# Optimization experiments

Measured on AMD Instinct MI355X. Metric: run time of the kernel, lower is better.

The kernel has to match this reference:

```python
import jax, jax.numpy as jnp
import numpy as np

B, H, N, D, S = 32, 4, 8192, 64, 3
EPS = 1e-10


def setup_inputs() -> dict:
    key = jax.random.key(0)
    ks = jax.random.split(key, 9)
    dev = 1.0 / np.sqrt(D + N)  # init scale from initialize_memory()
    memory = jax.random.uniform(ks[0], (B, N, D), minval=-dev, maxval=dev, dtype=jnp.float32)
    k = jax.random.normal(ks[1], (B, H, D), dtype=jnp.float32)
    beta = jax.random.uniform(ks[2], (B, H), dtype=jnp.float32) * 5.0          # key strength >= 0
    pw = jax.nn.softmax(jax.random.normal(ks[3], (B, H, N), dtype=jnp.float32), axis=-1)  # prev weights: simplex
    g = jax.random.uniform(ks[4], (B, H), dtype=jnp.float32)                    # gate in [0,1]
    s = jax.nn.softmax(jax.random.normal(ks[5], (B, H, S), dtype=jnp.float32), axis=-1)   # shift distribution
    gamma = 1.0 + 2.0 * jax.random.uniform(ks[6], (B, H), dtype=jnp.float32)    # sharpening >= 1
    erase = jax.random.uniform(ks[7], (B, H, D), dtype=jnp.float32)             # erase in [0,1]
    add = jax.random.normal(ks[8], (B, H, D), dtype=jnp.float32)
    return {"memory": memory, "k": k, "beta": beta, "pw": pw, "g": g,
            "s": s, "gamma": gamma, "erase": erase, "add": add}


def _ntm_step(memory, k, beta, pw, g, s, gamma, erase, add):
    # --- content addressing: softmax over slots of beta * cosine similarity ---
    kn = k / (jnp.linalg.norm(k, axis=-1, keepdims=True) + EPS)         # [B,H,D]
    mn = memory / (jnp.linalg.norm(memory, axis=-1, keepdims=True) + EPS)  # [B,N,D]
    cos = jnp.einsum('bhd,bnd->bhn', kn, mn)                            # [B,H,N]
    wc = jax.nn.softmax(beta[..., None] * cos, axis=-1)
    # --- location addressing: interpolate, circular shift, sharpen ---
    gb = g[..., None]
    wg = gb * wc + (1.0 - gb) * pw                                      # [B,H,N]
    center = (s.shape[-1] - 1) // 2
    # ws(i) = sum_j wg((i - off_j) mod N) * s(j), off_j = j - center
    ws = sum(s[..., j:j + 1] * jnp.roll(wg, j - center, axis=-1)
             for j in range(s.shape[-1]))
    wgam = ws ** gamma[..., None]
    w = wgam / jnp.sum(wgam, axis=-1, keepdims=True)                    # [B,H,N]
    # --- write: sequential erase/add outer products per head ---
    mem = memory
    for h in range(w.shape[1]):
        e = w[:, h, :, None] * erase[:, h, None, :]                     # [B,N,D]
        a = w[:, h, :, None] * add[:, h, None, :]
        mem = mem * (1.0 - e) + a
    # --- read from updated memory ---
    reading = jnp.einsum('bhn,bnd->bhd', w, mem)                        # [B,H,D]
    return reading


def reference(memory, k, beta, pw, g, s, gamma, erase, add):
    return _ntm_step(memory, k, beta, pw, g, s, gamma, erase, add)
```

## Files before the change

### kernel.cpp

```cpp
#include <hip/hip_runtime.h>
#include <math.h>

#define Bc 32
#define Hc 4
#define Nc 8192
#define Dc 64
#define EPSc 1e-10f

#define T1ROWS 64
#define NT1 (Nc / T1ROWS)
#define T2ROWS 256
#define NT2 (Nc / T2ROWS)
#define T3ROWS 128
#define NT3 (Nc / T3ROWS)

__global__ __launch_bounds__(256) void k_scores(
    const float* __restrict__ mem, const float* __restrict__ kk,
    const float* __restrict__ beta,
    float* __restrict__ tbuf, float* __restrict__ z1p)
{
    const int b = blockIdx.y, tile = blockIdx.x, tid = threadIdx.x;
    const int wave = tid >> 6, lane = tid & 63;

    __shared__ float ks[Hc][Dc];
    __shared__ float wsum[4][Hc];

    {
        float kv = kk[(b * Hc + wave) * Dc + lane];
        float ss = kv * kv;
        #pragma unroll
        for (int off = 32; off; off >>= 1) ss += __shfl_xor(ss, off);
        float scale = beta[b * Hc + wave] / (sqrtf(ss) + EPSc);
        ks[wave][lane] = kv * scale;
    }
    __syncthreads();

    const int r    = tid >> 2;
    const int part = tid & 3;
    const int n    = tile * T1ROWS + r;
    const float4* p4 = reinterpret_cast<const float4*>(
        mem + ((size_t)b * Nc + n) * Dc + part * 16);

    float ss = 0.f;
    float dot[Hc] = {0.f, 0.f, 0.f, 0.f};
    #pragma unroll
    for (int j = 0; j < 4; ++j) {
        float4 v = p4[j];
        ss = fmaf(v.x, v.x, ss); ss = fmaf(v.y, v.y, ss);
        ss = fmaf(v.z, v.z, ss); ss = fmaf(v.w, v.w, ss);
        const int c0 = part * 16 + 4 * j;
        #pragma unroll
        for (int h = 0; h < Hc; ++h) {
            dot[h] = fmaf(v.x, ks[h][c0 + 0], dot[h]);
            dot[h] = fmaf(v.y, ks[h][c0 + 1], dot[h]);
            dot[h] = fmaf(v.z, ks[h][c0 + 2], dot[h]);
            dot[h] = fmaf(v.w, ks[h][c0 + 3], dot[h]);
        }
    }
    #pragma unroll
    for (int off = 1; off <= 2; off <<= 1) {
        ss += __shfl_xor(ss, off);
        #pragma unroll
        for (int h = 0; h < Hc; ++h) dot[h] += __shfl_xor(dot[h], off);
    }
    const float inv = 1.0f / (sqrtf(ss) + EPSc);

    const float tval = __expf(dot[part] * inv);
    tbuf[(b * Hc + part) * Nc + n] = tval;

    float v = tval;
    #pragma unroll
    for (int off = 4; off <= 32; off <<= 1) v += __shfl_xor(v, off);
    if (lane < Hc) wsum[wave][lane] = v;
    __syncthreads();
    if (tid < Hc)
        z1p[(b * Hc + tid) * NT1 + tile] =
            wsum[0][tid] + wsum[1][tid] + wsum[2][tid] + wsum[3][tid];
}

__global__ __launch_bounds__(256) void k_shift(
    const float* __restrict__ tbuf, const float* __restrict__ z1p,
    const float* __restrict__ pw, const float* __restrict__ g,
    const float* __restrict__ s, const float* __restrict__ gamma,
    float* __restrict__ wgbuf, float* __restrict__ z2p,
    float* __restrict__ out)
{
    const int b = blockIdx.y, tile = blockIdx.x, tid = threadIdx.x;
    const int h = tid >> 6, lane = tid & 63;

    if (tile == 0) out[b * 256 + tid] = 0.f;

    float v = z1p[(b * Hc + h) * NT1 + lane] + z1p[(b * Hc + h) * NT1 + lane + 64];
    #pragma unroll
    for (int off = 32; off; off >>= 1) v += __shfl_xor(v, off);
    const float invZ1 = __shfl(1.0f / v, 0);

    const float gh  = g[b * Hc + h];
    const float gmh = gamma[b * Hc + h];
    const float s0 = s[(b * Hc + h) * 3 + 0];
    const float s1 = s[(b * Hc + h) * 3 + 1];
    const float s2 = s[(b * Hc + h) * 3 + 2];
    const float omg = 1.0f - gh;

    const int n0   = tile * T2ROWS + lane * 4;
    const int base = (b * Hc + h) * Nc;
    const int nm = (n0 == 0) ? (Nc - 1) : (n0 - 1);
    const int np = (n0 + 4 == Nc) ? 0 : (n0 + 4);

    const float4 t4  = *reinterpret_cast<const float4*>(tbuf + base + n0);
    const float4 p4  = *reinterpret_cast<const float4*>(pw   + base + n0);
    const float  tm = tbuf[base + nm], pm = pw[base + nm];
    const float  tp = tbuf[base + np], pp = pw[base + np];

    const float wgm1 = gh * tm   * invZ1 + omg * pm;
    const float wg0  = gh * t4.x * invZ1 + omg * p4.x;
    const float wg1  = gh * t4.y * invZ1 + omg * p4.y;
    const float wg2  = gh * t4.z * invZ1 + omg * p4.z;
    const float wg3  = gh * t4.w * invZ1 + omg * p4.w;
    const float wg4  = gh * tp   * invZ1 + omg * pp;

    float4 wgam;
    wgam.x = __powf(s0 * wg1 + s1 * wg0 + s2 * wgm1, gmh);
    wgam.y = __powf(s0 * wg2 + s1 * wg1 + s2 * wg0,  gmh);
    wgam.z = __powf(s0 * wg3 + s1 * wg2 + s2 * wg1,  gmh);
    wgam.w = __powf(s0 * wg4 + s1 * wg3 + s2 * wg2,  gmh);
    *reinterpret_cast<float4*>(wgbuf + base + n0) = wgam;

    float pv = wgam.x + wgam.y + wgam.z + wgam.w;
    #pragma unroll
    for (int off = 32; off; off >>= 1) pv += __shfl_xor(pv, off);
    if (lane == 0) z2p[(b * Hc + h) * NT2 + tile] = pv;
}

__global__ __launch_bounds__(256) void k_update(
    const float* __restrict__ mem, const float* __restrict__ wgbuf,
    const float* __restrict__ z2p, const float* __restrict__ erase,
    const float* __restrict__ add, float* __restrict__ out)
{
    const int b = blockIdx.y, tile = blockIdx.x, tid = threadIdx.x;
    const int part = tid & 15;
    const int rw   = tid >> 4;

    __shared__ float invZ2[Hc];
    {
        const int wave = tid >> 6, lane = tid & 63;
        float v = (lane < NT2) ? z2p[(b * Hc + wave) * NT2 + lane] : 0.f;
        #pragma unroll
        for (int off = 32; off; off >>= 1) v += __shfl_xor(v, off);
        if (lane == 0) invZ2[wave] = 1.0f / v;
    }
    __syncthreads();

    float4 e4[Hc], a4[Hc];
    float iz[Hc];
    #pragma unroll
    for (int h = 0; h < Hc; ++h) {
        e4[h] = *reinterpret_cast<const float4*>(erase + (b * Hc + h) * Dc + part * 4);
        a4[h] = *reinterpret_cast<const float4*>(add   + (b * Hc + h) * Dc + part * 4);
        iz[h] = invZ2[h];
    }

    float4 r4[Hc];
    #pragma unroll
    for (int h = 0; h < Hc; ++h) r4[h] = make_float4(0.f, 0.f, 0.f, 0.f);

    const int n0 = tile * T3ROWS;
    #pragma unroll 4
    for (int i = 0; i < T3ROWS / 16; ++i) {
        const int n = n0 + i * 16 + rw;
        float4 m4 = *reinterpret_cast<const float4*>(
            mem + ((size_t)b * Nc + n) * Dc + part * 4);
        float w[Hc];
        #pragma unroll
        for (int h = 0; h < Hc; ++h)
            w[h] = wgbuf[(b * Hc + h) * Nc + n] * iz[h];
        #pragma unroll
        for (int h = 0; h < Hc; ++h) {
            m4.x = m4.x * (1.0f - w[h] * e4[h].x) + w[h] * a4[h].x;
            m4.y = m4.y * (1.0f - w[h] * e4[h].y) + w[h] * a4[h].y;
            m4.z = m4.z * (1.0f - w[h] * e4[h].z) + w[h] * a4[h].z;
            m4.w = m4.w * (1.0f - w[h] * e4[h].w) + w[h] * a4[h].w;
        }
        #pragma unroll
        for (int h = 0; h < Hc; ++h) {
            r4[h].x = fmaf(w[h], m4.x, r4[h].x);
            r4[h].y = fmaf(w[h], m4.y, r4[h].y);
            r4[h].z = fmaf(w[h], m4.z, r4[h].z);
            r4[h].w = fmaf(w[h], m4.w, r4[h].w);
        }
    }

    __shared__ float4 acc[16][Hc][16];
    #pragma unroll
    for (int h = 0; h < Hc; ++h) acc[rw][h][part] = r4[h];
    __syncthreads();

    const int h = tid >> 6, d = tid & 63;
    float sum = 0.f;
    #pragma unroll
    for (int r2 = 0; r2 < 16; ++r2)
        sum += reinterpret_cast<const float*>(&acc[r2][h][d >> 2])[d & 3];
    atomicAdd(out + b * 256 + h * 64 + d, sum);
}

extern "C" void kernel_launch(void* const* d_in, const int* in_sizes, int n_in,
                              void* d_out, int out_size, void* d_ws, size_t ws_size,
                              hipStream_t stream) {
    const float* mem   = (const float*)d_in[0];
    const float* kk    = (const float*)d_in[1];
    const float* beta  = (const float*)d_in[2];
    const float* pw    = (const float*)d_in[3];
    const float* g     = (const float*)d_in[4];
    const float* s     = (const float*)d_in[5];
    const float* gamma = (const float*)d_in[6];
    const float* erase = (const float*)d_in[7];
    const float* add   = (const float*)d_in[8];
    float* out = (float*)d_out;

    float* ws    = (float*)d_ws;
    float* tbuf  = ws;
    float* wgbuf = tbuf + (size_t)Bc*Hc*Nc;
    float* z1p   = wgbuf + (size_t)Bc*Hc*Nc;
    float* z2p   = z1p + (size_t)Bc*Hc*NT1;

    k_scores<<<dim3(NT1, Bc), 256, 0, stream>>>(mem, kk, beta, tbuf, z1p);
    k_shift <<<dim3(NT2, Bc), 256, 0, stream>>>(tbuf, z1p, pw, g, s, gamma, wgbuf, z2p, out);
    k_update<<<dim3(NT3, Bc), 256, 0, stream>>>(mem, wgbuf, z2p, erase, add, out);
}
```

Baseline: 42.01 us.

## Restructure score kernel to coalesced 16-lane rows with register-cached keys

The content-scoring kernel now gives each 16-thread group one memory row per pass, with each thread reading one float4 and looping over 8 passes of 16 rows. Key vectors are held in registers instead of being re-read from shared memory on every use. Each block covers 128 rows, so there are half as many blocks and the partial-sum array shrinks to match, and the shift kernel reads a single partial per lane. The cross-lane reduction now takes four shuffle steps per row instead of two, and only 4 of 16 lanes write each score, which adds shuffle work and leaves most lanes idle at the store.

```diff
diff --git a/kernel.cpp b/kernel.cpp
--- a/kernel.cpp
+++ b/kernel.cpp
@@ -7,7 +7,7 @@
 #define Dc 64
 #define EPSc 1e-10f
 
-#define T1ROWS 64
+#define T1ROWS 128
 #define NT1 (Nc / T1ROWS)
 #define T2ROWS 256
 #define NT2 (Nc / T2ROWS)
@@ -21,6 +21,8 @@
 {
     const int b = blockIdx.y, tile = blockIdx.x, tid = threadIdx.x;
     const int wave = tid >> 6, lane = tid & 63;
+    const int col  = tid & 15;
+    const int rloc = tid >> 4;
 
     __shared__ float ks[Hc][Dc];
     __shared__ float wsum[4][Hc];
@@ -35,43 +37,50 @@
     }
     __syncthreads();
 
-    const int r    = tid >> 2;
-    const int part = tid & 3;
-    const int n    = tile * T1ROWS + r;
-    const float4* p4 = reinterpret_cast<const float4*>(
-        mem + ((size_t)b * Nc + n) * Dc + part * 16);
-
-    float ss = 0.f;
-    float dot[Hc] = {0.f, 0.f, 0.f, 0.f};
-    #pragma unroll
-    for (int j = 0; j < 4; ++j) {
-        float4 v = p4[j];
-        ss = fmaf(v.x, v.x, ss); ss = fmaf(v.y, v.y, ss);
-        ss = fmaf(v.z, v.z, ss); ss = fmaf(v.w, v.w, ss);
-        const int c0 = part * 16 + 4 * j;
+    float ksr[Hc][4];
+    #pragma unroll
+    for (int h = 0; h < Hc; ++h) {
+        ksr[h][0] = ks[h][col * 4 + 0];
+        ksr[h][1] = ks[h][col * 4 + 1];
+        ksr[h][2] = ks[h][col * 4 + 2];
+        ksr[h][3] = ks[h][col * 4 + 3];
+    }
+
+    float psum = 0.f;
+
+    #pragma unroll
+    for (int pass = 0; pass < T1ROWS / 16; ++pass) {
+        const int n = tile * T1ROWS + pass * 16 + rloc;
+        const float4 v = *reinterpret_cast<const float4*>(
+            mem + ((size_t)b * Nc + n) * Dc + col * 4);
+
+        float ss = v.x * v.x;
+        ss = fmaf(v.y, v.y, ss); ss = fmaf(v.z, v.z, ss); ss = fmaf(v.w, v.w, ss);
+        float dot[Hc];
         #pragma unroll
         for (int h = 0; h < Hc; ++h) {
-            dot[h] = fmaf(v.x, ks[h][c0 + 0], dot[h]);
-            dot[h] = fmaf(v.y, ks[h][c0 + 1], dot[h]);
-            dot[h] = fmaf(v.z, ks[h][c0 + 2], dot[h]);
-            dot[h] = fmaf(v.w, ks[h][c0 + 3], dot[h]);
-        }
-    }
-    #pragma unroll
-    for (int off = 1; off <= 2; off <<= 1) {
-        ss += __shfl_xor(ss, off);
-        #pragma unroll
-        for (int h = 0; h < Hc; ++h) dot[h] += __shfl_xor(dot[h], off);
-    }
-    const float inv = 1.0f / (sqrtf(ss) + EPSc);
-
-    const float tval = __expf(dot[part] * inv);
-    tbuf[(b * Hc + part) * Nc + n] = tval;
-
-    float v = tval;
-    #pragma unroll
-    for (int off = 4; off <= 32; off <<= 1) v += __shfl_xor(v, off);
-    if (lane < Hc) wsum[wave][lane] = v;
+            dot[h] = v.x * ksr[h][0];
+            dot[h] = fmaf(v.y, ksr[h][1], dot[h]);
+            dot[h] = fmaf(v.z, ksr[h][2], dot[h]);
+            dot[h] = fmaf(v.w, ksr[h][3], dot[h]);
+        }
+        #pragma unroll
+        for (int off = 1; off <= 8; off <<= 1) {
+            ss += __shfl_xor(ss, off);
+            #pragma unroll
+            for (int h = 0; h < Hc; ++h) dot[h] += __shfl_xor(dot[h], off);
+        }
+        const float inv  = 1.0f / (sqrtf(ss) + EPSc);
+        const float tval = __expf(dot[col & 3] * inv);
+        if (col < Hc) {
+            tbuf[(b * Hc + col) * Nc + n] = tval;
+            psum += tval;
+        }
+    }
+
+    #pragma unroll
+    for (int off = 16; off <= 32; off <<= 1) psum += __shfl_xor(psum, off);
+    if (lane < Hc) wsum[wave][lane] = psum;
     __syncthreads();
     if (tid < Hc)
         z1p[(b * Hc + tid) * NT1 + tile] =
@@ -90,7 +99,7 @@
 
     if (tile == 0) out[b * 256 + tid] = 0.f;
 
-    float v = z1p[(b * Hc + h) * NT1 + lane] + z1p[(b * Hc + h) * NT1 + lane + 64];
+    float v = z1p[(b * Hc + h) * NT1 + lane];
     #pragma unroll
     for (int off = 32; off; off >>= 1) v += __shfl_xor(v, off);
     const float invZ1 = __shfl(1.0f / v, 0);
```

Result: slower. 45.71 us (+8.8%).

## Stage memory rows through swizzled LDS so each thread owns one row in k_scores

Applied to the files above, without the earlier changes.

k_scores now processes 256 rows per block. Each thread computes the full row norm and all four head dot products for one row, reading it from a swizzled shared-memory staging buffer loaded in two coalesced halves. This removes the cross-lane shuffle reductions per row and the idle per-part exp/store work, and cuts the block count fourfold. The partial-sum count drops to 32, so k_shift reads it with a guard. The cost is 32KB of LDS per block and fewer blocks, which may lower occupancy and latency hiding.

```diff
diff --git a/kernel.cpp b/kernel.cpp
--- a/kernel.cpp
+++ b/kernel.cpp
@@ -7,7 +7,7 @@
 #define Dc 64
 #define EPSc 1e-10f
 
-#define T1ROWS 64
+#define T1ROWS 256
 #define NT1 (Nc / T1ROWS)
 #define T2ROWS 256
 #define NT2 (Nc / T2ROWS)
@@ -21,8 +21,10 @@
 {
     const int b = blockIdx.y, tile = blockIdx.x, tid = threadIdx.x;
     const int wave = tid >> 6, lane = tid & 63;
-
-    __shared__ float ks[Hc][Dc];
+    const int n0 = tile * T1ROWS;
+
+    __shared__ __align__(16) float ks[Hc][Dc];
+    __shared__ float4 lrow4[T1ROWS * 8];
     __shared__ float wsum[4][Hc];
 
     {
@@ -35,43 +37,56 @@
     }
     __syncthreads();
 
-    const int r    = tid >> 2;
-    const int part = tid & 3;
-    const int n    = tile * T1ROWS + r;
-    const float4* p4 = reinterpret_cast<const float4*>(
-        mem + ((size_t)b * Nc + n) * Dc + part * 16);
-
-    float ss = 0.f;
+    const float4* mem4 = reinterpret_cast<const float4*>(mem) + ((size_t)b * Nc + n0) * 16;
+
+    float ssacc = 0.f;
     float dot[Hc] = {0.f, 0.f, 0.f, 0.f};
-    #pragma unroll
-    for (int j = 0; j < 4; ++j) {
-        float4 v = p4[j];
-        ss = fmaf(v.x, v.x, ss); ss = fmaf(v.y, v.y, ss);
-        ss = fmaf(v.z, v.z, ss); ss = fmaf(v.w, v.w, ss);
-        const int c0 = part * 16 + 4 * j;
-        #pragma unroll
-        for (int h = 0; h < Hc; ++h) {
-            dot[h] = fmaf(v.x, ks[h][c0 + 0], dot[h]);
-            dot[h] = fmaf(v.y, ks[h][c0 + 1], dot[h]);
-            dot[h] = fmaf(v.z, ks[h][c0 + 2], dot[h]);
-            dot[h] = fmaf(v.w, ks[h][c0 + 3], dot[h]);
-        }
-    }
-    #pragma unroll
-    for (int off = 1; off <= 2; off <<= 1) {
-        ss += __shfl_xor(ss, off);
-        #pragma unroll
-        for (int h = 0; h < Hc; ++h) dot[h] += __shfl_xor(dot[h], off);
-    }
-    const float inv = 1.0f / (sqrtf(ss) + EPSc);
-
-    const float tval = __expf(dot[part] * inv);
-    tbuf[(b * Hc + part) * Nc + n] = tval;
-
-    float v = tval;
-    #pragma unroll
-    for (int off = 4; off <= 32; off <<= 1) v += __shfl_xor(v, off);
-    if (lane < Hc) wsum[wave][lane] = v;
+
+    #pragma unroll
+    for (int hf = 0; hf < 2; ++hf) {
+        if (hf) __syncthreads();
+
+        #pragma unroll
+        for (int k = 0; k < 8; ++k) {
+            const int f = k * 256 + tid;
+            const int r = f >> 3, sp = f & 7;
+            const int c = sp ^ (r & 7);
+            lrow4[f] = mem4[r * 16 + hf * 8 + c];
+        }
+        __syncthreads();
+
+        const float4* ks4 = reinterpret_cast<const float4*>(&ks[0][0]);
+        #pragma unroll
+        for (int c = 0; c < 8; ++c) {
+            const float4 v = lrow4[tid * 8 + (c ^ (tid & 7))];
+            ssacc = fmaf(v.x, v.x, ssacc); ssacc = fmaf(v.y, v.y, ssacc);
+            ssacc = fmaf(v.z, v.z, ssacc); ssacc = fmaf(v.w, v.w, ssacc);
+            #pragma unroll
+            for (int h = 0; h < Hc; ++h) {
+                const float4 kf = ks4[h * 16 + hf * 8 + c];
+                dot[h] = fmaf(v.x, kf.x, dot[h]);
+                dot[h] = fmaf(v.y, kf.y, dot[h]);
+                dot[h] = fmaf(v.z, kf.z, dot[h]);
+                dot[h] = fmaf(v.w, kf.w, dot[h]);
+            }
+        }
+    }
+
+    const float inv = 1.0f / (sqrtf(ssacc) + EPSc);
+    float psum[Hc];
+    #pragma unroll
+    for (int h = 0; h < Hc; ++h) {
+        const float tv = __expf(dot[h] * inv);
+        tbuf[(b * Hc + h) * Nc + n0 + tid] = tv;
+        psum[h] = tv;
+    }
+
+    #pragma unroll
+    for (int h = 0; h < Hc; ++h) {
+        #pragma unroll
+        for (int off = 32; off; off >>= 1) psum[h] += __shfl_xor(psum[h], off);
+        if (lane == 0) wsum[wave][h] = psum[h];
+    }
     __syncthreads();
     if (tid < Hc)
         z1p[(b * Hc + tid) * NT1 + tile] =
@@ -90,7 +105,7 @@
 
     if (tile == 0) out[b * 256 + tid] = 0.f;
 
-    float v = z1p[(b * Hc + h) * NT1 + lane] + z1p[(b * Hc + h) * NT1 + lane + 64];
+    float v = (lane < NT1) ? z1p[(b * Hc + h) * NT1 + lane] : 0.f;
     #pragma unroll
     for (int off = 32; off; off >>= 1) v += __shfl_xor(v, off);
     const float invZ1 = __shfl(1.0f / v, 0);
@@ -224,6 +239,7 @@
     float* z2p   = z1p + (size_t)Bc*Hc*NT1;
 
     k_scores<<<dim3(NT1, Bc), 256, 0, stream>>>(mem, kk, beta, tbuf, z1p);
-    k_shift <<<dim3(NT2, Bc), 256, 0, stream>>>(tbuf, z1p, pw, g, s, gamma, wgbuf, z2p, out);
+    k_shift <<<dim3(NT2, Bc), 256, 0, stream>>>(tbuf, z1p, pw, g, s, gamma,
+                                                wgbuf, z2p, out);
     k_update<<<dim3(NT3, Bc), 256, 0, stream>>>(mem, wgbuf, z2p, erase, add, out);
 }
```

After: 41.52 us, median of 3. About the same (-1.2%).
